# Kernel optimization log

Measured on AMD Instinct MI355X. Metric: run time of the kernel, lower is better.

The kernel has to match this reference:

```python
import jax, jax.numpy as jnp
import numpy as np

NUM_HEADS = 4
SCALE = 1.0  # source: self.scale = qkv_bias or head_dim**-0.5 -> True -> 1.0


def setup_inputs() -> dict:
    key = jax.random.key(0)
    ks = jax.random.split(key, 6)
    B_, N, C = 4096, 49, 128
    nW = 64
    return {
        "x": jax.random.normal(ks[0], (B_, N, C), dtype=jnp.float32),
        "mask": jax.random.normal(ks[1], (nW, N, N), dtype=jnp.float32),
        "w_qkv": jax.random.normal(ks[2], (C, 3 * C), dtype=jnp.float32) * (C ** -0.5),
        "b_qkv": jax.random.normal(ks[3], (3 * C,), dtype=jnp.float32) * 0.02,
        "w_proj": jax.random.normal(ks[4], (C, C), dtype=jnp.float32) * (C ** -0.5),
        "b_proj": jax.random.normal(ks[5], (C,), dtype=jnp.float32) * 0.02,
    }


def reference(x, mask, w_qkv, b_qkv, w_proj, b_proj):
    B_, N, C = x.shape
    H = NUM_HEADS
    hd = C // H
    # fused qkv projection: (B_, N, 3, H, hd) -> (3, B_, H, N, hd)
    qkv = (x @ w_qkv + b_qkv).reshape(B_, N, 3, H, hd).transpose(2, 0, 3, 1, 4)
    q, k, v = qkv[0], qkv[1], qkv[2]
    q = q * SCALE
    # per-window attention logits: (B_, H, N, N)
    attn = jnp.einsum("bhnd,bhmd->bhnm", q, k)
    nW = mask.shape[0]
    # additive window mask bias broadcast over batch and heads
    attn = attn.reshape(B_ // nW, nW, H, N, N) + mask[None, :, None, :, :]
    attn = jax.nn.softmax(attn, axis=-1).reshape(B_, H, N, N)
    out = jnp.einsum("bhnm,bhmd->bhnd", attn, v)  # (B_, H, N, hd)
    out = out.transpose(0, 2, 1, 3).reshape(B_, N, C)
    return out @ w_proj + b_proj
```

## Files before the change

kernel.cpp:

```cpp
#include <hip/hip_runtime.h>
#include <hip/hip_bf16.h>

typedef __attribute__((ext_vector_type(4))) float f32x4;
typedef _Float16 f16;
typedef __attribute__((ext_vector_type(8))) f16 f16x8;
typedef __attribute__((ext_vector_type(4))) f16 f16x4;
typedef __attribute__((ext_vector_type(2))) __fp16 fp16x2;

#define LDQ 136

#define GLOAD16(g, l)                                              \
  __builtin_amdgcn_global_load_lds(                                \
      (const __attribute__((address_space(1))) void*)(g),          \
      (__attribute__((address_space(3))) void*)(l), 16, 0, 0)

__global__ void pack_w_kernel(const float* __restrict__ w, f16* __restrict__ dst, int Ntot) {
  int idx = blockIdx.x * 256 + threadIdx.x;
  int total = (Ntot / 16) * 4 * 64;
  if (idx >= total) return;
  int lane = idx & 63;
  int kf = (idx >> 6) & 3;
  int nt = idx >> 8;
  int k0 = 32 * kf + 8 * (lane >> 4);
  int n = 16 * nt + (lane & 15);
  f16x8 v;
#pragma unroll
  for (int e = 0; e < 8; e++) v[e] = (f16)w[(k0 + e) * Ntot + n];
  *(f16x8*)(dst + (size_t)idx * 8) = v;
}

__global__ void pack_mask_kernel(const float* __restrict__ mask, float* __restrict__ dst) {
  int idx = blockIdx.x * 256 + threadIdx.x;
  int v = idx & 63;
  int l = (idx >> 6) & 63;
  int w = idx >> 12;
  int r = v & 3, mt = (v >> 2) & 3, nt = v >> 4;
  int q = 16 * nt + (l & 15);
  int key = 16 * mt + 4 * (l >> 4) + r;
  float val;
  if (key >= 49) val = -1e30f;
  else if (q < 49) val = mask[w * 2401 + q * 49 + key];
  else val = 0.f;
  dst[idx] = val;
}

__device__ __forceinline__ f16x4 pack4(f32x4 v) {
  union { f16x4 o; fp16x2 h[2]; } u;
  u.h[0] = __builtin_amdgcn_cvt_pkrtz(v[0], v[1]);
  u.h[1] = __builtin_amdgcn_cvt_pkrtz(v[2], v[3]);
  return u.o;
}

__device__ __forceinline__ f16x8 afrag(const float* xs, int row, int g0) {
  const f32x4 lo = *(const f32x4*)(xs + (((row << 5) + (g0 ^ (row & 7))) << 2));
  const f32x4 hi = *(const f32x4*)(xs + (((row << 5) + ((g0 + 1) ^ (row & 7))) << 2));
  union { f16x8 v; fp16x2 h[4]; } u;
  u.h[0] = __builtin_amdgcn_cvt_pkrtz(lo[0], lo[1]);
  u.h[1] = __builtin_amdgcn_cvt_pkrtz(lo[2], lo[3]);
  u.h[2] = __builtin_amdgcn_cvt_pkrtz(hi[0], hi[1]);
  u.h[3] = __builtin_amdgcn_cvt_pkrtz(hi[2], hi[3]);
  return u.v;
}

template <bool PM>
__global__ __launch_bounds__(256, 3) void winattn_fused(
    const float* __restrict__ x, const float* __restrict__ mask,
    const float* __restrict__ mask_p,
    const float* __restrict__ bqkv, const float* __restrict__ bproj,
    const f16* __restrict__ wqkv_p, const f16* __restrict__ wproj_p,
    float* __restrict__ out) {
  __shared__ float xs[64 * 128];
  __shared__ float msk[64 * 64];
  f16* Os = (f16*)xs;

  const int tid = threadIdx.x;
  const int h = tid >> 6;
  const int l = tid & 63;
  const int lg = l >> 4;
  const int ll = l & 15;
  const int b = blockIdx.x;
  const float* xw = x + (size_t)b * 49 * 128;

#pragma unroll
  for (int i = 0; i < 8; i++) {
    int c = i * 256 + tid;
    int r = c >> 5, s = c & 31;
    float* lp = xs + c * 4;
    if (r < 49) {
      GLOAD16(xw + r * 128 + ((s ^ (r & 7)) << 2), lp);
    } else {
      *(f32x4*)lp = (f32x4){0.f, 0.f, 0.f, 0.f};
    }
  }
  if (PM) {
    const float* mw = mask_p + ((size_t)(b & 63)) * 64 * 64;
#pragma unroll
    for (int i = 0; i < 4; i++) {
      int c = i * 256 + tid;
      int l2 = c >> 4, j = c & 15;
      GLOAD16(mw + l2 * 64 + ((j ^ (l2 & 15)) << 2), msk + c * 4);
    }
  }
  __syncthreads();

  f16x4 qv[2][4];
  {
    f32x4 acc[2][4];
#pragma unroll
    for (int mi = 0; mi < 2; mi++)
#pragma unroll
      for (int t = 0; t < 4; t++) acc[mi][t] = (f32x4){0.f, 0.f, 0.f, 0.f};
#pragma unroll
    for (int kst = 0; kst < 4; kst++) {
      f16x8 wf0 = *(const f16x8*)(wqkv_p + (size_t)((((2 * h + 0) * 4 + kst) * 64) + l) * 8);
      f16x8 wf1 = *(const f16x8*)(wqkv_p + (size_t)((((2 * h + 1) * 4 + kst) * 64) + l) * 8);
#pragma unroll
      for (int t = 0; t < 4; t++) {
        f16x8 a = afrag(xs, 16 * t + ll, 8 * kst + 2 * lg);
        acc[0][t] = __builtin_amdgcn_mfma_f32_16x16x32_f16(wf0, a, acc[0][t], 0, 0, 0);
        acc[1][t] = __builtin_amdgcn_mfma_f32_16x16x32_f16(wf1, a, acc[1][t], 0, 0, 0);
      }
    }
#pragma unroll
    for (int mi = 0; mi < 2; mi++) {
      f32x4 bq = *(const f32x4*)(bqkv + 16 * (2 * h + mi) + 4 * lg);
#pragma unroll
      for (int t = 0; t < 4; t++) {
        f32x4 a = acc[mi][t];
#pragma unroll
        for (int r = 0; r < 4; r++) a[r] += bq[r];
        qv[mi][t] = pack4(a);
      }
    }
  }

  f16x4 kv[2][4];
  {
    f32x4 acc[2][4];
#pragma unroll
    for (int mi = 0; mi < 2; mi++)
#pragma unroll
      for (int t = 0; t < 4; t++) acc[mi][t] = (f32x4){0.f, 0.f, 0.f, 0.f};
#pragma unroll
    for (int kst = 0; kst < 4; kst++) {
      f16x8 wf0 = *(const f16x8*)(wqkv_p + (size_t)((((8 + 2 * h + 0) * 4 + kst) * 64) + l) * 8);
      f16x8 wf1 = *(const f16x8*)(wqkv_p + (size_t)((((8 + 2 * h + 1) * 4 + kst) * 64) + l) * 8);
#pragma unroll
      for (int t = 0; t < 4; t++) {
        f16x8 a = afrag(xs, 16 * t + ll, 8 * kst + 2 * lg);
        acc[0][t] = __builtin_amdgcn_mfma_f32_16x16x32_f16(wf0, a, acc[0][t], 0, 0, 0);
        acc[1][t] = __builtin_amdgcn_mfma_f32_16x16x32_f16(wf1, a, acc[1][t], 0, 0, 0);
      }
    }
#pragma unroll
    for (int mi = 0; mi < 2; mi++) {
      f32x4 bk = *(const f32x4*)(bqkv + 16 * (8 + 2 * h + mi) + 4 * lg);
#pragma unroll
      for (int t = 0; t < 4; t++) {
        f32x4 a = acc[mi][t];
#pragma unroll
        for (int r = 0; r < 4; r++) a[r] += bk[r];
        kv[mi][t] = pack4(a);
      }
    }
  }

  f16x4 vv[2][4];
  {
    f32x4 acc[2][4];
#pragma unroll
    for (int vi = 0; vi < 2; vi++)
#pragma unroll
      for (int t = 0; t < 4; t++) acc[vi][t] = (f32x4){0.f, 0.f, 0.f, 0.f};
#pragma unroll
    for (int kst = 0; kst < 4; kst++) {
      f16x8 wf0 = *(const f16x8*)(wqkv_p + (size_t)((((16 + 2 * h + 0) * 4 + kst) * 64) + l) * 8);
      f16x8 wf1 = *(const f16x8*)(wqkv_p + (size_t)((((16 + 2 * h + 1) * 4 + kst) * 64) + l) * 8);
#pragma unroll
      for (int t = 0; t < 4; t++) {
        f16x8 a = afrag(xs, 16 * t + ll, 8 * kst + 2 * lg);
        acc[0][t] = __builtin_amdgcn_mfma_f32_16x16x32_f16(a, wf0, acc[0][t], 0, 0, 0);
        acc[1][t] = __builtin_amdgcn_mfma_f32_16x16x32_f16(a, wf1, acc[1][t], 0, 0, 0);
      }
    }
#pragma unroll
    for (int vi = 0; vi < 2; vi++) {
      float bv = bqkv[16 * (16 + 2 * h + vi) + ll];
#pragma unroll
      for (int t = 0; t < 4; t++) {
        f32x4 a = acc[vi][t];
#pragma unroll
        for (int r = 0; r < 4; r++) a[r] += bv;
        vv[vi][t] = pack4(a);
      }
    }
  }
  __syncthreads();

  const float* mk = mask + (size_t)(b & 63) * 49 * 49;
#pragma unroll
  for (int nt = 0; nt < 4; nt++) {
    f32x4 mv[4];
    if (PM) {
#pragma unroll
      for (int mt = 0; mt < 4; mt++)
        mv[mt] = *(const f32x4*)(msk + l * 64 + ((((nt << 2) + mt) ^ ll) << 2));
    }
    f32x4 s[4];
#pragma unroll
    for (int mt = 0; mt < 4; mt++) {
      f32x4 c0;
      if (PM) c0 = mv[mt];
      else c0 = (f32x4){0.f, 0.f, 0.f, 0.f};
      c0 = __builtin_amdgcn_mfma_f32_16x16x16f16(kv[0][mt], qv[0][nt], c0, 0, 0, 0);
      s[mt] = __builtin_amdgcn_mfma_f32_16x16x16f16(kv[1][mt], qv[1][nt], c0, 0, 0, 0);
    }
    if (!PM) {
#pragma unroll
      for (int mt = 0; mt < 4; mt++)
#pragma unroll
        for (int r = 0; r < 4; r++) {
          int q = 16 * nt + ll;
          int key = 16 * mt + 4 * lg + r;
          float add;
          if (key >= 49) add = -1e30f;
          else if (q < 49) add = mk[q * 49 + key];
          else add = 0.f;
          s[mt][r] += add;
        }
    }
#pragma unroll
    for (int mt = 0; mt < 4; mt++)
#pragma unroll
      for (int r = 0; r < 4; r++) s[mt][r] = __expf(s[mt][r]);
    float sum = (((s[0][0] + s[0][1]) + (s[0][2] + s[0][3])) +
                 ((s[1][0] + s[1][1]) + (s[1][2] + s[1][3]))) +
                (((s[2][0] + s[2][1]) + (s[2][2] + s[2][3])) +
                 ((s[3][0] + s[3][1]) + (s[3][2] + s[3][3])));
    sum += __shfl_xor(sum, 16);
    sum += __shfl_xor(sum, 32);
    float invn = __builtin_amdgcn_rcpf(sum);
    f16x4 pb[4];
#pragma unroll
    for (int mt = 0; mt < 4; mt++) {
      f32x4 pv;
#pragma unroll
      for (int r = 0; r < 4; r++) pv[r] = s[mt][r] * invn;
      pb[mt] = pack4(pv);
    }
#pragma unroll
    for (int mi = 0; mi < 2; mi++) {
      f32x4 o = {0.f, 0.f, 0.f, 0.f};
#pragma unroll
      for (int c = 0; c < 4; c++)
        o = __builtin_amdgcn_mfma_f32_16x16x16f16(vv[mi][c], pb[c], o, 0, 0, 0);
      *(f16x4*)(&Os[(16 * nt + ll) * LDQ + 32 * h + 16 * mi + 4 * lg]) = pack4(o);
    }
  }
  __syncthreads();

  f16x8 of[4][4];
#pragma unroll
  for (int nt = 0; nt < 4; nt++)
#pragma unroll
    for (int kst = 0; kst < 4; kst++)
      of[nt][kst] = *(const f16x8*)(&Os[(16 * nt + ll) * LDQ + 32 * kst + 8 * lg]);
#pragma unroll
  for (int moi = 0; moi < 2; moi++) {
    int mo = 2 * h + moi;
    f16x8 wf2[4];
#pragma unroll
    for (int kst = 0; kst < 4; kst++)
      wf2[kst] = *(const f16x8*)(wproj_p + (size_t)(((mo * 4 + kst) * 64) + l) * 8);
    f32x4 bp = *(const f32x4*)(bproj + 16 * mo + 4 * lg);
#pragma unroll
    for (int nt = 0; nt < 4; nt++) {
      f32x4 acc = {0.f, 0.f, 0.f, 0.f};
#pragma unroll
      for (int kst = 0; kst < 4; kst++)
        acc = __builtin_amdgcn_mfma_f32_16x16x32_f16(wf2[kst], of[nt][kst], acc, 0, 0, 0);
#pragma unroll
      for (int r = 0; r < 4; r++) acc[r] += bp[r];
      int tok = 16 * nt + ll;
      if (tok < 49)
        *(f32x4*)(&out[((size_t)b * 49 + tok) * 128 + 16 * mo + 4 * lg]) = acc;
    }
  }
}

extern "C" void kernel_launch(void* const* d_in, const int* in_sizes, int n_in,
                              void* d_out, int out_size, void* d_ws, size_t ws_size,
                              hipStream_t stream) {
  const float* x = (const float*)d_in[0];
  const float* mask = (const float*)d_in[1];
  const float* wqkv = (const float*)d_in[2];
  const float* bqkv = (const float*)d_in[3];
  const float* wproj = (const float*)d_in[4];
  const float* bproj = (const float*)d_in[5];
  float* out = (float*)d_out;

  f16* wqkv_p = (f16*)d_ws;
  f16* wproj_p = wqkv_p + 24 * 4 * 64 * 8;
  float* mask_p = (float*)((char*)d_ws + 128 * 1024);

  const size_t need_pm = 128 * 1024 + 1048576;

  pack_w_kernel<<<24, 256, 0, stream>>>(wqkv, wqkv_p, 384);
  pack_w_kernel<<<8, 256, 0, stream>>>(wproj, wproj_p, 128);

  if (ws_size >= need_pm) {
    pack_mask_kernel<<<1024, 256, 0, stream>>>(mask, mask_p);
    winattn_fused<true><<<4096, 256, 0, stream>>>(x, mask, mask_p, bqkv, bproj, wqkv_p, wproj_p, out);
  } else {
    winattn_fused<false><<<4096, 256, 0, stream>>>(x, mask, nullptr, bqkv, bproj, wqkv_p, wproj_p, out);
  }
}
```

Measured before the change: 84.97 us.

## Prefetch weight fragments earlier and fold log2e into Q and mask for exp2

Loads all QKV weight fragments for each projection up front and issues the output-projection weight and bias loads before the barrier, so global load latency overlaps with compute. It also pre-scales Q (and its bias) and the mask by log2(e), which lets the softmax use exp2f directly instead of __expf. More weight fragments stay live in registers, which could raise register pressure. Scaling Q before the fp16 conversion slightly changes rounding.

After: 85.14 us. Within noise of the previous version (+0.2%).

```diff
diff --git a/kernel.cpp b/kernel.cpp
--- a/kernel.cpp
+++ b/kernel.cpp
@@ -8,6 +8,7 @@
 typedef __attribute__((ext_vector_type(2))) __fp16 fp16x2;
 
 #define LDQ 136
+#define L2E 1.442695041f
 
 #define GLOAD16(g, l)                                              \
   __builtin_amdgcn_global_load_lds(                                \
@@ -41,7 +42,7 @@
   if (key >= 49) val = -1e30f;
   else if (q < 49) val = mask[w * 2401 + q * 49 + key];
   else val = 0.f;
-  dst[idx] = val;
+  dst[idx] = val * L2E;
 }
 
 __device__ __forceinline__ f16x4 pack4(f32x4 v) {
@@ -105,6 +106,13 @@
 
   f16x4 qv[2][4];
   {
+    f16x8 wf[8];
+#pragma unroll
+    for (int mi = 0; mi < 2; mi++)
+#pragma unroll
+      for (int kst = 0; kst < 4; kst++)
+        wf[mi * 4 + kst] =
+            *(const f16x8*)(wqkv_p + (size_t)((((2 * h + mi) * 4 + kst) * 64) + l) * 8);
     f32x4 acc[2][4];
 #pragma unroll
     for (int mi = 0; mi < 2; mi++)
@@ -112,23 +120,23 @@
       for (int t = 0; t < 4; t++) acc[mi][t] = (f32x4){0.f, 0.f, 0.f, 0.f};
 #pragma unroll
     for (int kst = 0; kst < 4; kst++) {
-      f16x8 wf0 = *(const f16x8*)(wqkv_p + (size_t)((((2 * h + 0) * 4 + kst) * 64) + l) * 8);
-      f16x8 wf1 = *(const f16x8*)(wqkv_p + (size_t)((((2 * h + 1) * 4 + kst) * 64) + l) * 8);
 #pragma unroll
       for (int t = 0; t < 4; t++) {
         f16x8 a = afrag(xs, 16 * t + ll, 8 * kst + 2 * lg);
-        acc[0][t] = __builtin_amdgcn_mfma_f32_16x16x32_f16(wf0, a, acc[0][t], 0, 0, 0);
-        acc[1][t] = __builtin_amdgcn_mfma_f32_16x16x32_f16(wf1, a, acc[1][t], 0, 0, 0);
+        acc[0][t] = __builtin_amdgcn_mfma_f32_16x16x32_f16(wf[kst], a, acc[0][t], 0, 0, 0);
+        acc[1][t] = __builtin_amdgcn_mfma_f32_16x16x32_f16(wf[4 + kst], a, acc[1][t], 0, 0, 0);
       }
     }
 #pragma unroll
     for (int mi = 0; mi < 2; mi++) {
       f32x4 bq = *(const f32x4*)(bqkv + 16 * (2 * h + mi) + 4 * lg);
 #pragma unroll
-      for (int t = 0; t < 4; t++) {
-        f32x4 a = acc[mi][t];
-#pragma unroll
-        for (int r = 0; r < 4; r++) a[r] += bq[r];
+      for (int r = 0; r < 4; r++) bq[r] *= L2E;
+#pragma unroll
+      for (int t = 0; t < 4; t++) {
+        f32x4 a;
+#pragma unroll
+        for (int r = 0; r < 4; r++) a[r] = fmaf(acc[mi][t][r], L2E, bq[r]);
         qv[mi][t] = pack4(a);
       }
     }
@@ -136,6 +144,13 @@
 
   f16x4 kv[2][4];
   {
+    f16x8 wf[8];
+#pragma unroll
+    for (int mi = 0; mi < 2; mi++)
+#pragma unroll
+      for (int kst = 0; kst < 4; kst++)
+        wf[mi * 4 + kst] =
+            *(const f16x8*)(wqkv_p + (size_t)((((8 + 2 * h + mi) * 4 + kst) * 64) + l) * 8);
     f32x4 acc[2][4];
 #pragma unroll
     for (int mi = 0; mi < 2; mi++)
@@ -143,13 +158,11 @@
       for (int t = 0; t < 4; t++) acc[mi][t] = (f32x4){0.f, 0.f, 0.f, 0.f};
 #pragma unroll
     for (int kst = 0; kst < 4; kst++) {
-      f16x8 wf0 = *(const f16x8*)(wqkv_p + (size_t)((((8 + 2 * h + 0) * 4 + kst) * 64) + l) * 8);
-      f16x8 wf1 = *(const f16x8*)(wqkv_p + (size_t)((((8 + 2 * h + 1) * 4 + kst) * 64) + l) * 8);
 #pragma unroll
       for (int t = 0; t < 4; t++) {
         f16x8 a = afrag(xs, 16 * t + ll, 8 * kst + 2 * lg);
-        acc[0][t] = __builtin_amdgcn_mfma_f32_16x16x32_f16(wf0, a, acc[0][t], 0, 0, 0);
-        acc[1][t] = __builtin_amdgcn_mfma_f32_16x16x32_f16(wf1, a, acc[1][t], 0, 0, 0);
+        acc[0][t] = __builtin_amdgcn_mfma_f32_16x16x32_f16(wf[kst], a, acc[0][t], 0, 0, 0);
+        acc[1][t] = __builtin_amdgcn_mfma_f32_16x16x32_f16(wf[4 + kst], a, acc[1][t], 0, 0, 0);
       }
     }
 #pragma unroll
@@ -167,6 +180,13 @@
 
   f16x4 vv[2][4];
   {
+    f16x8 wf[8];
+#pragma unroll
+    for (int vi = 0; vi < 2; vi++)
+#pragma unroll
+      for (int kst = 0; kst < 4; kst++)
+        wf[vi * 4 + kst] =
+            *(const f16x8*)(wqkv_p + (size_t)((((16 + 2 * h + vi) * 4 + kst) * 64) + l) * 8);
     f32x4 acc[2][4];
 #pragma unroll
     for (int vi = 0; vi < 2; vi++)
@@ -174,13 +194,11 @@
       for (int t = 0; t < 4; t++) acc[vi][t] = (f32x4){0.f, 0.f, 0.f, 0.f};
 #pragma unroll
     for (int kst = 0; kst < 4; kst++) {
-      f16x8 wf0 = *(const f16x8*)(wqkv_p + (size_t)((((16 + 2 * h + 0) * 4 + kst) * 64) + l) * 8);
-      f16x8 wf1 = *(const f16x8*)(wqkv_p + (size_t)((((16 + 2 * h + 1) * 4 + kst) * 64) + l) * 8);
 #pragma unroll
       for (int t = 0; t < 4; t++) {
         f16x8 a = afrag(xs, 16 * t + ll, 8 * kst + 2 * lg);
-        acc[0][t] = __builtin_amdgcn_mfma_f32_16x16x32_f16(a, wf0, acc[0][t], 0, 0, 0);
-        acc[1][t] = __builtin_amdgcn_mfma_f32_16x16x32_f16(a, wf1, acc[1][t], 0, 0, 0);
+        acc[0][t] = __builtin_amdgcn_mfma_f32_16x16x32_f16(a, wf[kst], acc[0][t], 0, 0, 0);
+        acc[1][t] = __builtin_amdgcn_mfma_f32_16x16x32_f16(a, wf[4 + kst], acc[1][t], 0, 0, 0);
       }
     }
 #pragma unroll
@@ -224,7 +242,7 @@
           int key = 16 * mt + 4 * lg + r;
           float add;
           if (key >= 49) add = -1e30f;
-          else if (q < 49) add = mk[q * 49 + key];
+          else if (q < 49) add = mk[q * 49 + key] * L2E;
           else add = 0.f;
           s[mt][r] += add;
         }
@@ -232,7 +250,7 @@
 #pragma unroll
     for (int mt = 0; mt < 4; mt++)
 #pragma unroll
-      for (int r = 0; r < 4; r++) s[mt][r] = __expf(s[mt][r]);
+      for (int r = 0; r < 4; r++) s[mt][r] = exp2f(s[mt][r]);
     float sum = (((s[0][0] + s[0][1]) + (s[0][2] + s[0][3])) +
                  ((s[1][0] + s[1][1]) + (s[1][2] + s[1][3]))) +
                 (((s[2][0] + s[2][1]) + (s[2][2] + s[2][3])) +
@@ -257,6 +275,17 @@
       *(f16x4*)(&Os[(16 * nt + ll) * LDQ + 32 * h + 16 * mi + 4 * lg]) = pack4(o);
     }
   }
+
+  f16x8 wf2[2][4];
+  f32x4 bp2[2];
+#pragma unroll
+  for (int moi = 0; moi < 2; moi++) {
+    int mo = 2 * h + moi;
+#pragma unroll
+    for (int kst = 0; kst < 4; kst++)
+      wf2[moi][kst] = *(const f16x8*)(wproj_p + (size_t)(((mo * 4 + kst) * 64) + l) * 8);
+    bp2[moi] = *(const f32x4*)(bproj + 16 * mo + 4 * lg);
+  }
   __syncthreads();
 
   f16x8 of[4][4];
@@ -268,19 +297,14 @@
 #pragma unroll
   for (int moi = 0; moi < 2; moi++) {
     int mo = 2 * h + moi;
-    f16x8 wf2[4];
-#pragma unroll
-    for (int kst = 0; kst < 4; kst++)
-      wf2[kst] = *(const f16x8*)(wproj_p + (size_t)(((mo * 4 + kst) * 64) + l) * 8);
-    f32x4 bp = *(const f32x4*)(bproj + 16 * mo + 4 * lg);
 #pragma unroll
     for (int nt = 0; nt < 4; nt++) {
       f32x4 acc = {0.f, 0.f, 0.f, 0.f};
 #pragma unroll
       for (int kst = 0; kst < 4; kst++)
-        acc = __builtin_amdgcn_mfma_f32_16x16x32_f16(wf2[kst], of[nt][kst], acc, 0, 0, 0);
-#pragma unroll
-      for (int r = 0; r < 4; r++) acc[r] += bp[r];
+        acc = __builtin_amdgcn_mfma_f32_16x16x32_f16(wf2[moi][kst], of[nt][kst], acc, 0, 0, 0);
+#pragma unroll
+      for (int r = 0; r < 4; r++) acc[r] += bp2[moi][r];
       int tok = 16 * nt + ll;
       if (tok < 49)
         *(f32x4*)(&out[((size_t)b * 49 + tok) * 128 + 16 * mo + 4 * lg]) = acc;
```
